# Performance work log

Measured on AMD Instinct MI355X. Metric: run time of the kernel, lower is better.

The kernel has to match this reference:

```python
import jax, jax.numpy as jnp
import numpy as np

K_GRAD = 20        # num_nbrs for gradient operator
K_NORMAL = 10      # knn for normal/basis estimation
GRAD_REG = 1e-3    # grad_reg (lambda)
KERNEL_WIDTH = 1.0 # grad_kernel_width
EPS = 1e-8
N1, N2 = 8192, 8192
CHANNELS = [3, 64, 128, 256]


def knn_idx(pos, k):
    # brute-force kNN incl. self (loop=True, target_to_source)
    sq = jnp.sum(pos * pos, axis=1)
    d2 = sq[:, None] + sq[None, :] - 2.0 * (pos @ pos.T)
    _, idx = jax.lax.top_k(-d2, k)
    return idx  # [N, k]


def estimate_basis(pos, nbr, orientation):
    rel = pos[nbr] - pos[:, None, :]              # [N,k,3]
    cov = jnp.einsum('nki,nkj->nij', rel, rel)    # [N,3,3] local PCA
    _, vecs = jnp.linalg.eigh(cov)                # ascending eigenvalues
    normal, x_basis = vecs[:, :, 0], vecs[:, :, 2]
    sign = jnp.where(jnp.sum(normal * orientation, -1, keepdims=True) < 0.0, -1.0, 1.0)
    normal = normal * sign                        # orient along `orientation`
    y_basis = jnp.cross(normal, x_basis)
    return normal, x_basis, y_basis


def build_grad_div(pos, x_basis, y_basis, nbr):
    # regularized, Gaussian-weighted least-squares fit of a linear function per neighborhood
    rel = pos[nbr] - pos[:, None, :]              # [N,k,3]
    u = jnp.einsum('nkd,nd->nk', rel, x_basis)    # tangent coords
    v = jnp.einsum('nkd,nd->nk', rel, y_basis)
    dist = jnp.sqrt(jnp.sum(rel * rel, -1) + EPS)
    h = jnp.mean(dist, axis=1, keepdims=True)     # per-point bandwidth
    w = jnp.exp(-(dist * dist) / ((KERNEL_WIDTH * h) ** 2 + EPS))
    B = jnp.stack([jnp.ones_like(u), u, v], -1)   # [N,k,3] design matrix
    BtW = jnp.swapaxes(B, 1, 2) * w[:, None, :]   # [N,3,k]
    A = BtW @ B + GRAD_REG * jnp.eye(3, dtype=pos.dtype)
    C = jnp.linalg.solve(A, BtW)                  # [N,3,k] LS coefficients
    Gx, Gy = C[:, 1, :], C[:, 2, :]               # gradient stencils
    basis = jnp.stack([x_basis, y_basis], -1)     # [N,3,2]
    R = jnp.einsum('nda,nkdb->nkab', basis, basis[nbr])  # transport j->i, [N,k,2,2]
    return Gx, Gy, R


def grad_apply(Gx, Gy, nbr, f):
    fn = f[nbr]                                   # [N,k,C]
    return jnp.stack([jnp.einsum('nk,nkc->nc', Gx, fn),
                      jnp.einsum('nk,nkc->nc', Gy, fn)], 1)  # [N,2,C]


def div_apply(Gx, Gy, R, nbr, v):
    vt = jnp.einsum('nkab,nkbc->nkac', R, v[nbr])  # transported neighbor vectors
    return (jnp.einsum('nk,nkc->nc', Gx, vt[:, :, 0]) +
            jnp.einsum('nk,nkc->nc', Gy, vt[:, :, 1]))


def delta_conv(x, v, nbr, Gx, Gy, R, Ws, bs, Wv, bv, centralized):
    xn = x[nbr]
    if centralized:
        xn = xn - x[:, None, :]
    xmax = jnp.max(xn, axis=1)                    # max aggregation
    dv = div_apply(Gx, Gy, R, nbr, v)             # divergence
    Jv = jnp.stack([-v[:, 1], v[:, 0]], 1)        # 90-degree rotation
    cv = div_apply(Gx, Gy, R, nbr, Jv)            # curl = div(J v)
    x_out = jax.nn.relu(jnp.concatenate([xmax, dv, cv], -1) @ Ws + bs)
    if Wv is None:
        return x_out, v                            # last layer: scalar only
    gv = grad_apply(Gx, Gy, nbr, x_out)           # [N,2,Cout]
    vo = jnp.concatenate([v, gv], -1) @ Wv        # channel mix, no bias (equivariant)
    n = jnp.sqrt(jnp.sum(vo * vo, axis=1, keepdims=True) + EPS)
    vo = vo * (jax.nn.relu(n + bv) / (n + EPS))   # norm-gated vector nonlinearity
    return x_out, vo


def _forward(points, als_ppoints, params):
    pos = jnp.concatenate([points, als_ppoints], axis=0)  # [N,3]
    nbr = knn_idx(pos, K_GRAD)
    nbr_n = knn_idx(pos, K_NORMAL)
    _, xb, yb = estimate_basis(pos, nbr_n, orientation=pos)
    Gx, Gy, R = build_grad_div(pos, xb, yb, nbr)
    x = pos
    v = grad_apply(Gx, Gy, nbr, x)                # v = grad @ x
    out = []
    for i, (Ws, bs, Wv, bv) in enumerate(params):
        x, v = delta_conv(x, v, nbr, Gx, Gy, R, Ws, bs, Wv, bv, centralized=(i == 0))
        out.append(x)
    return tuple(out)


def setup_inputs():
    key = jax.random.key(0)
    ks = jax.random.split(key, 8)
    inp = {
        'points': jax.random.normal(ks[0], (N1, 3), jnp.float32),
        'als_ppoints': jax.random.normal(ks[1], (N2, 3), jnp.float32),
    }
    ki = 2
    for i in range(3):
        cin, cout = CHANNELS[i], CHANNELS[i + 1]
        inp[f'Ws{i}'] = jax.random.normal(ks[ki], (3 * cin, cout), jnp.float32) / np.sqrt(3.0 * cin)
        inp[f'bs{i}'] = jnp.zeros((cout,), jnp.float32)
        ki += 1
        if i < 2:
            inp[f'Wv{i}'] = jax.random.normal(ks[ki], (cin + cout, cout), jnp.float32) / np.sqrt(float(cin + cout))
            inp[f'bv{i}'] = jnp.zeros((cout,), jnp.float32)
            ki += 1
    return inp


def reference(points, als_ppoints, Ws0, bs0, Wv0, bv0, Ws1, bs1, Wv1, bv1, Ws2, bs2):
    params = [(Ws0, bs0, Wv0, bv0), (Ws1, bs1, Wv1, bv1), (Ws2, bs2, None, None)]
    return _forward(points, als_ppoints, params)
```

## Files before the change

### kernel.cpp

```cpp
#include <hip/hip_runtime.h>
#include <math.h>

#define NPTS 16384
#define KG 20
#define KN 10
#define KC 6
#define EPSF 1e-8f

#define GDIM 32
#define GL 4.75f
#define CW 0.296875f
#define GINV 3.3684210526f
#define RMAX 6

typedef __attribute__((ext_vector_type(8))) short short8v;
typedef __attribute__((ext_vector_type(4))) float floatx4;

__device__ __forceinline__ unsigned short f2bf(float v) {
  union { float f; unsigned u; } x;
  x.f = v;
  unsigned r = x.u + 0x7FFFu + ((x.u >> 16) & 1u);
  return (unsigned short)(r >> 16);
}

__device__ __forceinline__ float bf2f(unsigned short u) {
  union { unsigned u32; float f; } x;
  x.u32 = (unsigned)u << 16;
  return x.f;
}

#define KNN_INSERT(d2v, iv)                                                 \
  if ((d2v) < dist[KG - 1]) {                                               \
    dist[KG - 1] = (d2v); idx[KG - 1] = (iv);                               \
    _Pragma("unroll")                                                       \
    for (int s_ = KG - 1; s_ > 0; --s_) {                                   \
      if (dist[s_] < dist[s_ - 1]) {                                        \
        float td_ = dist[s_]; dist[s_] = dist[s_ - 1]; dist[s_ - 1] = td_;  \
        int ti_ = idx[s_]; idx[s_] = idx[s_ - 1]; idx[s_ - 1] = ti_;        \
      }                                                                     \
    }                                                                       \
  }

#define KNN_INSERTC(d2v, iv)                                                \
  if ((d2v) < dist[KC - 1]) {                                               \
    dist[KC - 1] = (d2v); idx[KC - 1] = (iv);                               \
    _Pragma("unroll")                                                       \
    for (int s_ = KC - 1; s_ > 0; --s_) {                                   \
      if (dist[s_] < dist[s_ - 1]) {                                        \
        float td_ = dist[s_]; dist[s_] = dist[s_ - 1]; dist[s_ - 1] = td_;  \
        int ti_ = idx[s_]; idx[s_] = idx[s_ - 1]; idx[s_ - 1] = ti_;        \
      }                                                                     \
    }                                                                       \
  }

__device__ __forceinline__ int cell_of(float x) {
  int c = (int)floorf((x + GL) * GINV);
  return min(max(c, 0), GDIM - 1);
}

__global__ __launch_bounds__(256) void posbin_kernel(const float* __restrict__ pts,
                                                     const float* __restrict__ als,
                                                     float4* __restrict__ pos4,
                                                     int* __restrict__ cell_count,
                                                     int* __restrict__ pt_cell) {
  int n = blockIdx.x * 256 + threadIdx.x;
  if (n >= NPTS) return;
  const float* src = (n < 8192) ? (pts + (size_t)n * 3) : (als + (size_t)(n - 8192) * 3);
  float x = src[0], y = src[1], z = src[2];
  pos4[n] = make_float4(x, y, z, 0.f);
  int c = (cell_of(z) * GDIM + cell_of(y)) * GDIM + cell_of(x);
  pt_cell[n] = c;
  atomicAdd(&cell_count[c], 1);
}

__global__ __launch_bounds__(1024) void scan_kernel(const int* __restrict__ cell_count,
                                                    int* __restrict__ cell_start,
                                                    int* __restrict__ cell_cursor) {
  __shared__ int s[1024];
  int tid = threadIdx.x;
  int base = tid * 32;
  int local[32];
  int sum = 0;
#pragma unroll
  for (int i = 0; i < 32; ++i) { local[i] = cell_count[base + i]; sum += local[i]; }
  s[tid] = sum;
  __syncthreads();
  for (int off = 1; off < 1024; off <<= 1) {
    int v = (tid >= off) ? s[tid - off] : 0;
    __syncthreads();
    s[tid] += v;
    __syncthreads();
  }
  int run = s[tid] - sum;
#pragma unroll
  for (int i = 0; i < 32; ++i) {
    cell_start[base + i] = run;
    cell_cursor[base + i] = run;
    run += local[i];
  }
}

__global__ __launch_bounds__(256) void scatter_kernel(const float4* __restrict__ pos4,
                                                      const int* __restrict__ pt_cell,
                                                      int* __restrict__ cell_cursor,
                                                      float4* __restrict__ sorted4,
                                                      int* __restrict__ sortmap) {
  int i = blockIdx.x * 256 + threadIdx.x;
  if (i >= NPTS) return;
  int c = pt_cell[i];
  int dst = atomicAdd(&cell_cursor[c], 1);
  float4 p = pos4[i];
  p.w = __int_as_float(i);
  sorted4[dst] = p;
  sortmap[dst] = i;
}

__global__ __launch_bounds__(256) void knn_grid_kernel(const float4* __restrict__ sorted4,
                                                       const int* __restrict__ cell_start,
                                                       const int* __restrict__ cell_count,
                                                       int* __restrict__ nbr,
                                                       int* __restrict__ fb_list,
                                                       int* __restrict__ fb_count) {
  int lane = threadIdx.x & 63;
  int sub = lane >> 5;
  int sl = lane & 31;
  int qs = blockIdx.x * 8 + (threadIdx.x >> 6) * 2 + sub;
  if (qs >= NPTS) return;
  float4 p = sorted4[qs];
  int cx = cell_of(p.x), cy = cell_of(p.y), cz = cell_of(p.z);
  float dist[KC];
  int idx[KC];
#pragma unroll
  for (int i = 0; i < KC; ++i) { dist[i] = 3.4e38f; idx[i] = 0; }

  {
    int tot = 0;
    int x0 = max(cx - 1, 0), x1 = min(cx + 1, GDIM - 1);
    int zlo = max(cz - 1, 0), zhi = min(cz + 1, GDIM - 1);
    int ylo = max(cy - 1, 0), yhi = min(cy + 1, GDIM - 1);
    for (int z = zlo; z <= zhi; ++z) {
      for (int y = ylo; y <= yhi; ++y) {
        int c0 = (z * GDIM + y) * GDIM + x0;
        int c1 = (z * GDIM + y) * GDIM + x1;
        int beg = cell_start[c0];
        int end = cell_start[c1] + cell_count[c1];
        int off = (sl - tot) & 31;
        for (int j = beg + off; j < end; j += 32) {
          float4 sp = sorted4[j];
          float dx = sp.x - p.x, dy = sp.y - p.y, dz = sp.z - p.z;
          float d2 = dx * dx + dy * dy + dz * dz;
          KNN_INSERTC(d2, j);
        }
        tot += end - beg;
      }
    }
  }
  int done;
  {
    float b2 = CW * CW;
    int cnt = 0;
#pragma unroll
    for (int i = 0; i < KC; ++i) cnt += (dist[i] <= b2) ? 1 : 0;
#pragma unroll
    for (int s = 1; s < 32; s <<= 1) cnt += __shfl_xor(cnt, s, 64);
    done = (cnt >= KG) ? 1 : 0;
  }

  for (int r = 2; r <= RMAX && !done; ++r) {
    int side = 2 * r + 1;
    int nt = side * side;
    float rcp = 1.0f / (float)side;
    for (int t = sl; t < nt; t += 32) {
      int qz = (int)(((float)t + 0.5f) * rcp);
      int dz = qz - r;
      int dy = t - qz * side - r;
      int z = cz + dz, y = cy + dy;
      if (z < 0 || z >= GDIM || y < 0 || y >= GDIM) continue;
      int rowbase = (z * GDIM + y) * GDIM;
      if (dz == -r || dz == r || dy == -r || dy == r) {
        int xa = max(cx - r, 0), xb = min(cx + r, GDIM - 1);
        int beg = cell_start[rowbase + xa];
        int end = cell_start[rowbase + xb] + cell_count[rowbase + xb];
        for (int j = beg; j < end; ++j) {
          float4 sp = sorted4[j];
          float ddx = sp.x - p.x, ddy = sp.y - p.y, ddz = sp.z - p.z;
          float d2 = ddx * ddx + ddy * ddy + ddz * ddz;
          KNN_INSERTC(d2, j);
        }
      } else {
        int x = cx - r;
        if (x >= 0) {
          int c = rowbase + x;
          int beg = cell_start[c], end = beg + cell_count[c];
          for (int j = beg; j < end; ++j) {
            float4 sp = sorted4[j];
            float ddx = sp.x - p.x, ddy = sp.y - p.y, ddz = sp.z - p.z;
            float d2 = ddx * ddx + ddy * ddy + ddz * ddz;
            KNN_INSERTC(d2, j);
          }
        }
        x = cx + r;
        if (x < GDIM) {
          int c = rowbase + x;
          int beg = cell_start[c], end = beg + cell_count[c];
          for (int j = beg; j < end; ++j) {
            float4 sp = sorted4[j];
            float ddx = sp.x - p.x, ddy = sp.y - p.y, ddz = sp.z - p.z;
            float d2 = ddx * ddx + ddy * ddy + ddz * ddz;
            KNN_INSERTC(d2, j);
          }
        }
      }
    }
    float b = CW * (float)r;
    float b2 = b * b;
    int cnt = 0;
#pragma unroll
    for (int i = 0; i < KC; ++i) cnt += (dist[i] <= b2) ? 1 : 0;
#pragma unroll
    for (int s = 1; s < 32; s <<= 1) cnt += __shfl_xor(cnt, s, 64);
    if (cnt >= KG) done = 1;
  }

  int popc = 0, ovf = 0;
  for (int round = 0; round < KG; ++round) {
    unsigned long long key = ((unsigned long long)__float_as_uint(dist[0]) << 14) |
                             (unsigned long long)(unsigned)idx[0];
    unsigned long long m = key;
#pragma unroll
    for (int s = 1; s < 32; s <<= 1) {
      unsigned long long o = __shfl_xor(m, s, 64);
      if (o < m) m = o;
    }
    if (key == m) {
      nbr[(size_t)qs * KG + round] = (int)(m & 0x3FFF);
#pragma unroll
      for (int s = 0; s < KC - 1; ++s) { dist[s] = dist[s + 1]; idx[s] = idx[s + 1]; }
      dist[KC - 1] = 3.4e38f;
      idx[KC - 1] = 0;
      if (++popc == KC) ovf = 1;
    }
  }
#pragma unroll
  for (int s = 1; s < 32; s <<= 1) ovf |= __shfl_xor(ovf, s, 64);
  if ((ovf || !done) && sl == 0) {
    int s = atomicAdd(fb_count, 1);
    fb_list[s] = qs;
  }
}

__global__ __launch_bounds__(256) void knn_fb_kernel(const float4* __restrict__ sorted4,
                                                     const int* __restrict__ fb_list,
                                                     const int* __restrict__ fb_count,
                                                     int* __restrict__ nbr) {
  __shared__ unsigned long long lists[256 * KG];
  __shared__ unsigned long long heads[256];
  __shared__ unsigned long long winner;
  int tid = threadIdx.x;
  int cnt = *fb_count;
  for (int qi = blockIdx.x; qi < cnt; qi += gridDim.x) {
    int t = fb_list[qi];
    float4 p = sorted4[t];
    float dist[KG];
    int idx[KG];
#pragma unroll
    for (int i = 0; i < KG; ++i) { dist[i] = 3.4e38f; idx[i] = 0; }
    int j0 = tid * 64;
    for (int j = j0; j < j0 + 64; ++j) {
      float4 c = sorted4[j];
      float dx = c.x - p.x, dy = c.y - p.y, dz = c.z - p.z;
      float d2 = dx * dx + dy * dy + dz * dz;
      KNN_INSERT(d2, j);
    }
#pragma unroll
    for (int i = 0; i < KG; ++i)
      lists[tid * KG + i] = ((unsigned long long)__float_as_uint(dist[i]) << 22) |
                            ((unsigned long long)(unsigned)idx[i] << 8) |
                            (unsigned long long)tid;
    int hp = 0;
    __syncthreads();
    for (int round = 0; round < KG; ++round) {
      heads[tid] = (hp < KG) ? lists[tid * KG + hp] : ~0ull;
      __syncthreads();
      if (tid < 64) {
        unsigned long long m = heads[tid];
        unsigned long long o = heads[tid + 64];  if (o < m) m = o;
        o = heads[tid + 128]; if (o < m) m = o;
        o = heads[tid + 192]; if (o < m) m = o;
#pragma unroll
        for (int s = 32; s > 0; s >>= 1) {
          unsigned long long x = __shfl_xor(m, s, 64);
          if (x < m) m = x;
        }
        if (tid == 0) winner = m;
      }
      __syncthreads();
      unsigned long long w = winner;
      if (tid == (int)(w & 0xFF)) hp++;
      if (tid == 0) nbr[(size_t)t * KG + round] = (int)((w >> 8) & 0x3FFF);
      __syncthreads();
    }
  }
}

__global__ __launch_bounds__(256) void basis_kernel(const float4* __restrict__ sorted4,
                                                    const int* __restrict__ nbr,
                                                    float4* __restrict__ xb4,
                                                    float4* __restrict__ yb4) {
  int n = blockIdx.x * 256 + threadIdx.x;
  if (n >= NPTS) return;
  float4 p = sorted4[n];
  float c00 = 0, c01 = 0, c02 = 0, c11 = 0, c12 = 0, c22 = 0;
  for (int k = 0; k < KN; ++k) {
    int m = nbr[(size_t)n * KG + k];
    float4 pm = sorted4[m];
    float dx = pm.x - p.x, dy = pm.y - p.y, dz = pm.z - p.z;
    c00 += dx * dx; c01 += dx * dy; c02 += dx * dz;
    c11 += dy * dy; c12 += dy * dz; c22 += dz * dz;
  }
  float nx = 0.f, ny = 0.f, nz = 1.f;
  float p1 = c01 * c01 + c02 * c02 + c12 * c12;
  float qm = (c00 + c11 + c22) * (1.f / 3.f);
  float g0 = c00 - qm, g1 = c11 - qm, g2 = c22 - qm;
  float p2 = g0 * g0 + g1 * g1 + g2 * g2 + 2.f * p1;
  if (p2 > 1e-16f) {
    float pp = sqrtf(p2 * (1.f / 6.f));
    float inv = 1.f / pp;
    float b00 = g0 * inv, b11 = g1 * inv, b22 = g2 * inv;
    float b01 = c01 * inv, b02 = c02 * inv, b12 = c12 * inv;
    float detB = b00 * (b11 * b22 - b12 * b12) - b01 * (b01 * b22 - b12 * b02) +
                 b02 * (b01 * b12 - b11 * b02);
    float r = 0.5f * detB;
    r = fminf(1.f, fmaxf(-1.f, r));
    float phi = acosf(r) * (1.f / 3.f);
    float e1 = qm + 2.f * pp * __cosf(phi);
    float e3 = qm + 2.f * pp * __cosf(phi + 2.0943951023931953f);
    float e2 = 3.f * qm - e1 - e3;
    float a00 = c00 - e1, a11 = c11 - e1, a22 = c22 - e1;
    float f00 = c00 - e2, f11 = c11 - e2, f22 = c22 - e2;
    float u0 = a00 * f00 + c01 * c01 + c02 * c02;
    float u1 = c01 * f00 + a11 * c01 + c12 * c02;
    float u2 = c02 * f00 + c12 * c01 + a22 * c02;
    float v0 = a00 * c01 + c01 * f11 + c02 * c12;
    float v1 = c01 * c01 + a11 * f11 + c12 * c12;
    float v2 = c02 * c01 + c12 * f11 + a22 * c12;
    float w0 = a00 * c02 + c01 * c12 + c02 * f22;
    float w1 = c01 * c02 + a11 * c12 + c12 * f22;
    float w2 = c02 * c02 + c12 * c12 + a22 * f22;
    float nu = u0 * u0 + u1 * u1 + u2 * u2;
    float nv = v0 * v0 + v1 * v1 + v2 * v2;
    float nw = w0 * w0 + w1 * w1 + w2 * w2;
    float bx = u0, by = u1, bz = u2, bn = nu;
    if (nv > bn) { bx = v0; by = v1; bz = v2; bn = nv; }
    if (nw > bn) { bx = w0; by = w1; bz = w2; bn = nw; }
    if (bn > 1e-30f) {
      float s = 1.f / sqrtf(bn);
      nx = bx * s; ny = by * s; nz = bz * s;
    }
  }
  float dotp = nx * p.x + ny * p.y + nz * p.z;
  if (dotp < 0.f) { nx = -nx; ny = -ny; nz = -nz; }
  float ax = fabsf(nx), ay = fabsf(ny), az = fabsf(nz);
  float ex = 0.f, ey = 0.f, ez = 0.f;
  if (ax <= ay && ax <= az) ex = 1.f;
  else if (ay <= az) ey = 1.f;
  else ez = 1.f;
  float tx = ny * ez - nz * ey, ty = nz * ex - nx * ez, tz = nx * ey - ny * ex;
  float tn = 1.f / sqrtf(tx * tx + ty * ty + tz * tz);
  tx *= tn; ty *= tn; tz *= tn;
  float ux = ny * tz - nz * ty, uy = nz * tx - nx * tz, uz = nx * ty - ny * tx;
  xb4[n] = make_float4(tx, ty, tz, 0.f);
  yb4[n] = make_float4(ux, uy, uz, 0.f);
}

__global__ __launch_bounds__(256) void graddiv_kernel(const float4* __restrict__ sorted4,
                                                      const int* __restrict__ nbr,
                                                      const float4* __restrict__ xb4,
                                                      const float4* __restrict__ yb4,
                                                      float* __restrict__ Gx,
                                                      float* __restrict__ Gy,
                                                      float2* __restrict__ C2,
                                                      float* __restrict__ v0) {
  int n = blockIdx.x * 256 + threadIdx.x;
  if (n >= NPTS) return;
  float4 p = sorted4[n], xb = xb4[n], yb = yb4[n];
  float u[KG], vv[KG], w[KG];
  int mm[KG];
  float hsum = 0.f;
#pragma unroll
  for (int k = 0; k < KG; ++k) {
    int m = nbr[(size_t)n * KG + k];
    mm[k] = m;
    float4 pm = sorted4[m];
    float rx = pm.x - p.x, ry = pm.y - p.y, rz = pm.z - p.z;
    u[k] = rx * xb.x + ry * xb.y + rz * xb.z;
    vv[k] = rx * yb.x + ry * yb.y + rz * yb.z;
    float dd = sqrtf(rx * rx + ry * ry + rz * rz + EPSF);
    w[k] = dd; hsum += dd;
  }
  float h = hsum * (1.f / KG);
  float invden = 1.f / (h * h + EPSF);
  float A00 = 0, A01 = 0, A02 = 0, A11 = 0, A12 = 0, A22 = 0;
#pragma unroll
  for (int k = 0; k < KG; ++k) {
    float wk = __expf(-(w[k] * w[k]) * invden);
    w[k] = wk;
    A00 += wk; A01 += wk * u[k]; A02 += wk * vv[k];
    A11 += wk * u[k] * u[k]; A12 += wk * u[k] * vv[k];
    A22 += wk * vv[k] * vv[k];
  }
  A00 += 0.001f; A11 += 0.001f; A22 += 0.001f;
  float det = A00 * (A11 * A22 - A12 * A12) - A01 * (A01 * A22 - A12 * A02) +
              A02 * (A01 * A12 - A11 * A02);
  float idet = 1.f / det;
  float i10 = (A02 * A12 - A01 * A22) * idet;
  float i11 = (A00 * A22 - A02 * A02) * idet;
  float i12 = (A01 * A02 - A00 * A12) * idet;
  float i20 = (A01 * A12 - A02 * A11) * idet;
  float i21 = i12;
  float i22 = (A00 * A11 - A01 * A01) * idet;
  float a0x = 0, a0y = 0, a0z = 0, a1x = 0, a1y = 0, a1z = 0;
#pragma unroll
  for (int k = 0; k < KG; ++k) {
    float gx = w[k] * (i10 + i11 * u[k] + i12 * vv[k]);
    float gy = w[k] * (i20 + i21 * u[k] + i22 * vv[k]);
    Gx[(size_t)n * KG + k] = gx;
    Gy[(size_t)n * KG + k] = gy;
    int m = mm[k];
    float4 pm = sorted4[m];
    a0x += gx * pm.x; a0y += gx * pm.y; a0z += gx * pm.z;
    a1x += gy * pm.x; a1y += gy * pm.y; a1z += gy * pm.z;
    float4 xm = xb4[m], ym = yb4[m];
    float g3x = gx * xb.x + gy * yb.x;
    float g3y = gx * xb.y + gy * yb.y;
    float g3z = gx * xb.z + gy * yb.z;
    float ca = g3x * xm.x + g3y * xm.y + g3z * xm.z;
    float cb = g3x * ym.x + g3y * ym.y + g3z * ym.z;
    C2[(size_t)n * KG + k] = make_float2(ca, cb);
  }
  v0[((size_t)n * 2 + 0) * 3 + 0] = a0x;
  v0[((size_t)n * 2 + 0) * 3 + 1] = a0y;
  v0[((size_t)n * 2 + 0) * 3 + 2] = a0z;
  v0[((size_t)n * 2 + 1) * 3 + 0] = a1x;
  v0[((size_t)n * 2 + 1) * 3 + 1] = a1y;
  v0[((size_t)n * 2 + 1) * 3 + 2] = a1z;
}

template <int CENTRAL>
__global__ __launch_bounds__(256) void feat16_kernel(const float* __restrict__ x, int ldx,
                                                     int cin,
                                                     const float* __restrict__ v,
                                                     const int* __restrict__ nbr,
                                                     const float2* __restrict__ C2,
                                                     unsigned short* __restrict__ feat, int Kp) {
  int per = Kp - 2 * cin;
  int gid = blockIdx.x * 256 + threadIdx.x;
  if (gid >= NPTS * per) return;
  int n = gid / per;
  int c = gid - n * per;
  size_t fb = (size_t)n * Kp;
  if (c >= cin) {
    feat[fb + 3 * cin + (c - cin)] = 0;
    return;
  }
  float xc = x[(size_t)n * ldx + c];
  float xmax = -3.4e38f, dv = 0.f, cv = 0.f;
  for (int k = 0; k < KG; ++k) {
    int m = nbr[(size_t)n * KG + k];
    float2 cc = C2[(size_t)n * KG + k];
    float xm = x[(size_t)m * ldx + c];
    xmax = fmaxf(xmax, CENTRAL ? (xm - xc) : xm);
    float va = v[((size_t)m * 2 + 0) * cin + c];
    float vb = v[((size_t)m * 2 + 1) * cin + c];
    dv += cc.x * va + cc.y * vb;
    cv += cc.y * va - cc.x * vb;
  }
  feat[fb + c] = f2bf(xmax);
  feat[fb + cin + c] = f2bf(dv);
  feat[fb + 2 * cin + c] = f2bf(cv);
}

__global__ __launch_bounds__(256) void feat16v8_kernel(const unsigned short* __restrict__ x,
                                                       int cin,
                                                       const unsigned short* __restrict__ v,
                                                       const int* __restrict__ nbr,
                                                       const float2* __restrict__ C2,
                                                       unsigned short* __restrict__ feat) {
  int per = cin >> 3;
  int gid = blockIdx.x * 256 + threadIdx.x;
  if (gid >= NPTS * per) return;
  int n = gid / per;
  int c8 = (gid - n * per) << 3;
  float xmax[8], dv[8], cv[8];
#pragma unroll
  for (int i = 0; i < 8; ++i) { xmax[i] = -3.4e38f; dv[i] = 0.f; cv[i] = 0.f; }
  const int* nrow = nbr + (size_t)n * KG;
  const float2* crow = C2 + (size_t)n * KG;
#pragma unroll 4
  for (int k = 0; k < KG; ++k) {
    int m = nrow[k];
    float2 cc = crow[k];
    short8v xm = *reinterpret_cast<const short8v*>(x + (size_t)m * cin + c8);
    short8v va = *reinterpret_cast<const short8v*>(v + ((size_t)m * 2 + 0) * cin + c8);
    short8v vb = *reinterpret_cast<const short8v*>(v + ((size_t)m * 2 + 1) * cin + c8);
#pragma unroll
    for (int i = 0; i < 8; ++i) {
      float xf = bf2f((unsigned short)xm[i]);
      float af = bf2f((unsigned short)va[i]);
      float bf = bf2f((unsigned short)vb[i]);
      xmax[i] = fmaxf(xmax[i], xf);
      dv[i] += cc.x * af + cc.y * bf;
      cv[i] += cc.y * af - cc.x * bf;
    }
  }
  size_t fb = (size_t)n * (3 * cin);
  short8v o0, o1, o2;
#pragma unroll
  for (int i = 0; i < 8; ++i) {
    o0[i] = (short)f2bf(xmax[i]);
    o1[i] = (short)f2bf(dv[i]);
    o2[i] = (short)f2bf(cv[i]);
  }
  *reinterpret_cast<short8v*>(&feat[fb + c8]) = o0;
  *reinterpret_cast<short8v*>(&feat[fb + cin + c8]) = o1;
  *reinterpret_cast<short8v*>(&feat[fb + 2 * cin + c8]) = o2;
}

__global__ __launch_bounds__(256) void vin16_kernel(const float* __restrict__ v, int cin,
                                                    const unsigned short* __restrict__ xout,
                                                    int cout,
                                                    const int* __restrict__ nbr,
                                                    const float* __restrict__ Gx,
                                                    const float* __restrict__ Gy,
                                                    unsigned short* __restrict__ vinb, int Kp,
                                                    int total) {
  int gid = blockIdx.x * 256 + threadIdx.x;
  if (gid >= total) return;
  int n = gid / Kp;
  int c = gid - n * Kp;
  int K = cin + cout;
  unsigned short o0, o1;
  if (c < cin) {
    o0 = f2bf(v[((size_t)n * 2 + 0) * cin + c]);
    o1 = f2bf(v[((size_t)n * 2 + 1) * cin + c]);
  } else if (c < K) {
    int cc = c - cin;
    float a0 = 0.f, a1 = 0.f;
    for (int k = 0; k < KG; ++k) {
      int m = nbr[(size_t)n * KG + k];
      float f = bf2f(xout[(size_t)m * cout + cc]);
      a0 += Gx[(size_t)n * KG + k] * f;
      a1 += Gy[(size_t)n * KG + k] * f;
    }
    o0 = f2bf(a0);
    o1 = f2bf(a1);
  } else {
    o0 = 0; o1 = 0;
  }
  vinb[((size_t)n * 2 + 0) * Kp + c] = o0;
  vinb[((size_t)n * 2 + 1) * Kp + c] = o1;
}

__global__ __launch_bounds__(256) void vin16v8_kernel(const unsigned short* __restrict__ v,
                                                      int cin,
                                                      const unsigned short* __restrict__ xout,
                                                      int cout,
                                                      const int* __restrict__ nbr,
                                                      const float* __restrict__ Gx,
                                                      const float* __restrict__ Gy,
                                                      unsigned short* __restrict__ vinb,
                                                      int Kp) {
  int per = Kp >> 3;
  int gid = blockIdx.x * 256 + threadIdx.x;
  if (gid >= NPTS * per) return;
  int n = gid / per;
  int c8 = (gid - n * per) << 3;
  short8v o0, o1;
  if (c8 < cin) {
    o0 = *reinterpret_cast<const short8v*>(v + ((size_t)n * 2 + 0) * cin + c8);
    o1 = *reinterpret_cast<const short8v*>(v + ((size_t)n * 2 + 1) * cin + c8);
  } else {
    int cc8 = c8 - cin;
    float a0[8], a1[8];
#pragma unroll
    for (int i = 0; i < 8; ++i) { a0[i] = 0.f; a1[i] = 0.f; }
    const int* nrow = nbr + (size_t)n * KG;
    const float* gxr = Gx + (size_t)n * KG;
    const float* gyr = Gy + (size_t)n * KG;
#pragma unroll 4
    for (int k = 0; k < KG; ++k) {
      int m = nrow[k];
      float gx = gxr[k], gy = gyr[k];
      short8v f = *reinterpret_cast<const short8v*>(xout + (size_t)m * cout + cc8);
#pragma unroll
      for (int i = 0; i < 8; ++i) {
        float ff = bf2f((unsigned short)f[i]);
        a0[i] += gx * ff;
        a1[i] += gy * ff;
      }
    }
#pragma unroll
    for (int i = 0; i < 8; ++i) {
      o0[i] = (short)f2bf(a0[i]);
      o1[i] = (short)f2bf(a1[i]);
    }
  }
  *reinterpret_cast<short8v*>(&vinb[((size_t)n * 2 + 0) * Kp + c8]) = o0;
  *reinterpret_cast<short8v*>(&vinb[((size_t)n * 2 + 1) * Kp + c8]) = o1;
}

__device__ __forceinline__ void wprep_one(const float* W, unsigned short* Wt, int K, int Kp,
                                          int N, int i) {
  int n = i / Kp, k = i - n * Kp;
  Wt[i] = (k < K) ? f2bf(W[(size_t)k * N + n]) : (unsigned short)0;
}

__global__ __launch_bounds__(256) void wprep_all_kernel(const float* __restrict__ Ws0,
                                                        const float* __restrict__ Wv0,
                                                        const float* __restrict__ Ws1,
                                                        const float* __restrict__ Wv1,
                                                        const float* __restrict__ Ws2,
                                                        unsigned short* __restrict__ Wt_s0,
                                                        unsigned short* __restrict__ Wt_v0,
                                                        unsigned short* __restrict__ Wt_s1,
                                                        unsigned short* __restrict__ Wt_v1,
                                                        unsigned short* __restrict__ Wt_s2) {
  int gid = blockIdx.x * 256 + threadIdx.x;
  if (gid < 2048) wprep_one(Ws0, Wt_s0, 9, 32, 64, gid);
  else if (gid < 8192) wprep_one(Wv0, Wt_v0, 67, 96, 64, gid - 2048);
  else if (gid < 32768) wprep_one(Ws1, Wt_s1, 192, 192, 128, gid - 8192);
  else if (gid < 57344) wprep_one(Wv1, Wt_v1, 192, 192, 128, gid - 32768);
  else if (gid < 155648) wprep_one(Ws2, Wt_s2, 384, 384, 256, gid - 57344);
}

template <int MODE>
__global__ __launch_bounds__(256) void gemm16_kernel(const unsigned short* __restrict__ A,
                                                     const unsigned short* __restrict__ Bt,
                                                     const float* __restrict__ bias,
                                                     float* __restrict__ Cf,
                                                     unsigned short* __restrict__ Cb,
                                                     const int* __restrict__ rowmap,
                                                     int Kp, int Ncol) {
  int lane = threadIdx.x & 63;
  int wave = threadIdx.x >> 6;
  int rowBase = blockIdx.y * 64 + wave * 16;
  int colBase = blockIdx.x * 64;
  int lr = lane & 15;
  int kg = (lane >> 4) * 8;
  floatx4 acc0 = {0.f, 0.f, 0.f, 0.f};
  floatx4 acc1 = acc0, acc2 = acc0, acc3 = acc0;
  const unsigned short* arow = A + (size_t)(rowBase + lr) * Kp + kg;
  const unsigned short* b0p = Bt + (size_t)(colBase + lr) * Kp + kg;
  for (int k0 = 0; k0 < Kp; k0 += 32) {
    short8v a = *reinterpret_cast<const short8v*>(arow + k0);
    short8v b0 = *reinterpret_cast<const short8v*>(b0p + k0);
    short8v b1 = *reinterpret_cast<const short8v*>(b0p + (size_t)16 * Kp + k0);
    short8v b2 = *reinterpret_cast<const short8v*>(b0p + (size_t)32 * Kp + k0);
    short8v b3 = *reinterpret_cast<const short8v*>(b0p + (size_t)48 * Kp + k0);
    acc0 = __builtin_amdgcn_mfma_f32_16x16x32_bf16(a, b0, acc0, 0, 0, 0);
    acc1 = __builtin_amdgcn_mfma_f32_16x16x32_bf16(a, b1, acc1, 0, 0, 0);
    acc2 = __builtin_amdgcn_mfma_f32_16x16x32_bf16(a, b2, acc2, 0, 0, 0);
    acc3 = __builtin_amdgcn_mfma_f32_16x16x32_bf16(a, b3, acc3, 0, 0, 0);
  }
  int rsub = (lane >> 4) * 4;
  floatx4 accs[4] = {acc0, acc1, acc2, acc3};
  int orow[4];
  if (MODE == 0) {
#pragma unroll
    for (int r = 0; r < 4; ++r) orow[r] = rowmap[rowBase + rsub + r];
  }
#pragma unroll
  for (int nb = 0; nb < 4; ++nb) {
    int col = colBase + nb * 16 + lr;
    float bb = bias[col];
    if (MODE == 0) {
#pragma unroll
      for (int r = 0; r < 4; ++r) {
        int row = rowBase + rsub + r;
        float val = fmaxf(accs[nb][r] + bb, 0.f);
        Cf[(size_t)orow[r] * Ncol + col] = val;
        if (Cb) Cb[(size_t)row * Ncol + col] = f2bf(val);
      }
    } else {
#pragma unroll
      for (int pr = 0; pr < 2; ++pr) {
        float a0 = accs[nb][2 * pr], a1 = accs[nb][2 * pr + 1];
        float nrm = sqrtf(a0 * a0 + a1 * a1 + EPSF);
        float s = fmaxf(nrm + bb, 0.f) / (nrm + EPSF);
        int row = rowBase + rsub + 2 * pr;
        Cb[(size_t)row * Ncol + col] = f2bf(a0 * s);
        Cb[(size_t)(row + 1) * Ncol + col] = f2bf(a1 * s);
      }
    }
  }
}

extern "C" void kernel_launch(void* const* d_in, const int* in_sizes, int n_in,
                              void* d_out, int out_size, void* d_ws, size_t ws_size,
                              hipStream_t stream) {
  const float* pts = (const float*)d_in[0];
  const float* als = (const float*)d_in[1];
  const float* Ws0 = (const float*)d_in[2];
  const float* bs0 = (const float*)d_in[3];
  const float* Wv0 = (const float*)d_in[4];
  const float* bv0 = (const float*)d_in[5];
  const float* Ws1 = (const float*)d_in[6];
  const float* bs1 = (const float*)d_in[7];
  const float* Wv1 = (const float*)d_in[8];
  const float* bv1 = (const float*)d_in[9];
  const float* Ws2 = (const float*)d_in[10];
  const float* bs2 = (const float*)d_in[11];

  char* ws = (char*)d_ws;
  float4* pos4 = (float4*)(ws + 0);
  int* nbr = (int*)(ws + 262144);
  float4* xb4 = (float4*)(ws + 1572864);
  float4* yb4 = (float4*)(ws + 1835008);
  float* Gx = (float*)(ws + 2097152);
  float* Gy = (float*)(ws + 3407872);
  float2* C2 = (float2*)(ws + 4718592);
  float* v0f = (float*)(ws + 7340032);
  unsigned short* vb_a = (unsigned short*)(ws + 8388608);
  unsigned short* vb_b = (unsigned short*)(ws + 17825792);
  unsigned short* xb0m = (unsigned short*)(ws + 23068672);
  unsigned short* xb1m = (unsigned short*)(ws + 26214400);
  unsigned short* stg = (unsigned short*)(ws + 31457280);
  char* wtb = ws + 45088768;
  unsigned short* Wt_s0 = (unsigned short*)(wtb + 0);
  unsigned short* Wt_v0 = (unsigned short*)(wtb + 4096);
  unsigned short* Wt_s1 = (unsigned short*)(wtb + 16384);
  unsigned short* Wt_v1 = (unsigned short*)(wtb + 65536);
  unsigned short* Wt_s2 = (unsigned short*)(wtb + 114688);

  char* gws = ws + 46137344;
  int* cell_count = (int*)(gws + 0);
  int* fb_count = (int*)(gws + 131072);
  int* cell_start = (int*)(gws + 135168);
  int* cell_cursor = (int*)(gws + 266240);
  int* pt_cell = (int*)(gws + 397312);
  int* fb_list = (int*)(gws + 462848);
  float4* sorted4 = (float4*)(gws + 532480);
  int* sortmap = (int*)(gws + 794624);

  float* out0 = (float*)d_out;
  float* out1 = out0 + (size_t)NPTS * 64;
  float* out2 = out1 + (size_t)NPTS * 128;

  hipMemsetAsync(cell_count, 0, 131072 + 4, stream);
  posbin_kernel<<<64, 256, 0, stream>>>(pts, als, pos4, cell_count, pt_cell);
  scan_kernel<<<1, 1024, 0, stream>>>(cell_count, cell_start, cell_cursor);
  scatter_kernel<<<64, 256, 0, stream>>>(pos4, pt_cell, cell_cursor, sorted4, sortmap);
  knn_grid_kernel<<<NPTS / 8, 256, 0, stream>>>(sorted4, cell_start, cell_count, nbr, fb_list,
                                                fb_count);
  knn_fb_kernel<<<128, 256, 0, stream>>>(sorted4, fb_list, fb_count, nbr);

  basis_kernel<<<64, 256, 0, stream>>>(sorted4, nbr, xb4, yb4);
  graddiv_kernel<<<64, 256, 0, stream>>>(sorted4, nbr, xb4, yb4, Gx, Gy, C2, v0f);

  wprep_all_kernel<<<608, 256, 0, stream>>>(Ws0, Wv0, Ws1, Wv1, Ws2, Wt_s0, Wt_v0, Wt_s1,
                                            Wt_v1, Wt_s2);

  feat16_kernel<1><<<(NPTS * 26 + 255) / 256, 256, 0, stream>>>((const float*)sorted4, 4, 3,
                                                                v0f, nbr, C2, stg, 32);
  gemm16_kernel<0><<<dim3(1, 256), 256, 0, stream>>>(stg, Wt_s0, bs0, out0, xb0m, sortmap, 32,
                                                     64);
  vin16_kernel<<<(NPTS * 96 + 255) / 256, 256, 0, stream>>>(v0f, 3, xb0m, 64, nbr, Gx, Gy, stg,
                                                            96, NPTS * 96);
  gemm16_kernel<1><<<dim3(1, 512), 256, 0, stream>>>(stg, Wt_v0, bv0, nullptr, vb_b, nullptr,
                                                     96, 64);

  feat16v8_kernel<<<NPTS * 8 / 256, 256, 0, stream>>>(xb0m, 64, vb_b, nbr, C2, stg);
  gemm16_kernel<0><<<dim3(2, 256), 256, 0, stream>>>(stg, Wt_s1, bs1, out1, xb1m, sortmap, 192,
                                                     128);
  vin16v8_kernel<<<NPTS * 24 / 256, 256, 0, stream>>>(vb_b, 64, xb1m, 128, nbr, Gx, Gy, stg,
                                                      192);
  gemm16_kernel<1><<<dim3(2, 512), 256, 0, stream>>>(stg, Wt_v1, bv1, nullptr, vb_a, nullptr,
                                                     192, 128);

  feat16v8_kernel<<<NPTS * 16 / 256, 256, 0, stream>>>(xb1m, 128, vb_a, nbr, C2, stg);
  gemm16_kernel<0><<<dim3(4, 256), 256, 0, stream>>>(stg, Wt_s2, bs2, out2, nullptr, sortmap,
                                                     384, 256);
}
```

Baseline: 292.0 us.

## Fuse weight prep into posbin, unroll kNN scan by two, stage neighbors in LDS

Merges the weight-transpose/bf16 conversion kernel into the point-binning kernel, which removes one launch. Unrolls the grid kNN candidate loop to process two candidates per iteration so more loads are in flight. In feat16v8, a block's neighbor indices and coefficients are loaded cooperatively into shared memory, so threads sharing a point no longer issue redundant global loads. The changes add a __syncthreads and some per-thread branch divergence in the fused kernel.

```diff
diff --git a/kernel.cpp b/kernel.cpp
--- a/kernel.cpp
+++ b/kernel.cpp
@@ -58,19 +58,37 @@
   return min(max(c, 0), GDIM - 1);
 }
 
-__global__ __launch_bounds__(256) void posbin_kernel(const float* __restrict__ pts,
-                                                     const float* __restrict__ als,
-                                                     float4* __restrict__ pos4,
-                                                     int* __restrict__ cell_count,
-                                                     int* __restrict__ pt_cell) {
-  int n = blockIdx.x * 256 + threadIdx.x;
-  if (n >= NPTS) return;
-  const float* src = (n < 8192) ? (pts + (size_t)n * 3) : (als + (size_t)(n - 8192) * 3);
-  float x = src[0], y = src[1], z = src[2];
-  pos4[n] = make_float4(x, y, z, 0.f);
-  int c = (cell_of(z) * GDIM + cell_of(y)) * GDIM + cell_of(x);
-  pt_cell[n] = c;
-  atomicAdd(&cell_count[c], 1);
+__device__ __forceinline__ void wprep_one(const float* W, unsigned short* Wt, int K, int Kp,
+                                          int N, int i) {
+  int n = i / Kp, k = i - n * Kp;
+  Wt[i] = (k < K) ? f2bf(W[(size_t)k * N + n]) : (unsigned short)0;
+}
+
+__global__ __launch_bounds__(256) void posbin_wprep_kernel(
+    const float* __restrict__ pts, const float* __restrict__ als, float4* __restrict__ pos4,
+    int* __restrict__ cell_count, int* __restrict__ pt_cell,
+    const float* __restrict__ Ws0, const float* __restrict__ Wv0,
+    const float* __restrict__ Ws1, const float* __restrict__ Wv1,
+    const float* __restrict__ Ws2, unsigned short* __restrict__ Wt_s0,
+    unsigned short* __restrict__ Wt_v0, unsigned short* __restrict__ Wt_s1,
+    unsigned short* __restrict__ Wt_v1, unsigned short* __restrict__ Wt_s2) {
+  if (blockIdx.x < 64) {
+    int n = blockIdx.x * 256 + threadIdx.x;
+    if (n >= NPTS) return;
+    const float* src = (n < 8192) ? (pts + (size_t)n * 3) : (als + (size_t)(n - 8192) * 3);
+    float x = src[0], y = src[1], z = src[2];
+    pos4[n] = make_float4(x, y, z, 0.f);
+    int c = (cell_of(z) * GDIM + cell_of(y)) * GDIM + cell_of(x);
+    pt_cell[n] = c;
+    atomicAdd(&cell_count[c], 1);
+  } else {
+    int gid = (blockIdx.x - 64) * 256 + threadIdx.x;
+    if (gid < 2048) wprep_one(Ws0, Wt_s0, 9, 32, 64, gid);
+    else if (gid < 8192) wprep_one(Wv0, Wt_v0, 67, 96, 64, gid - 2048);
+    else if (gid < 32768) wprep_one(Ws1, Wt_s1, 192, 192, 128, gid - 8192);
+    else if (gid < 57344) wprep_one(Wv1, Wt_v1, 192, 192, 128, gid - 32768);
+    else if (gid < 155648) wprep_one(Ws2, Wt_s2, 384, 384, 256, gid - 57344);
+  }
 }
 
 __global__ __launch_bounds__(1024) void scan_kernel(const int* __restrict__ cell_count,
@@ -145,11 +163,16 @@
         int beg = cell_start[c0];
         int end = cell_start[c1] + cell_count[c1];
         int off = (sl - tot) & 31;
-        for (int j = beg + off; j < end; j += 32) {
-          float4 sp = sorted4[j];
-          float dx = sp.x - p.x, dy = sp.y - p.y, dz = sp.z - p.z;
-          float d2 = dx * dx + dy * dy + dz * dz;
-          KNN_INSERTC(d2, j);
+        for (int j = beg + off; j < end; j += 64) {
+          int j1 = j + 32;
+          float4 sp0 = sorted4[j];
+          float4 sp1 = sorted4[(j1 < end) ? j1 : j];
+          float dx0 = sp0.x - p.x, dy0 = sp0.y - p.y, dz0 = sp0.z - p.z;
+          float d20 = dx0 * dx0 + dy0 * dy0 + dz0 * dz0;
+          float dx1 = sp1.x - p.x, dy1 = sp1.y - p.y, dz1 = sp1.z - p.z;
+          float d21 = dx1 * dx1 + dy1 * dy1 + dz1 * dz1;
+          KNN_INSERTC(d20, j);
+          if (j1 < end) { KNN_INSERTC(d21, j1); }
         }
         tot += end - beg;
       }
@@ -486,16 +509,27 @@
                                                        const int* __restrict__ nbr,
                                                        const float2* __restrict__ C2,
                                                        unsigned short* __restrict__ feat) {
+  __shared__ int s_nbr[32 * KG];
+  __shared__ float2 s_c2[32 * KG];
   int per = cin >> 3;
-  int gid = blockIdx.x * 256 + threadIdx.x;
-  if (gid >= NPTS * per) return;
-  int n = gid / per;
-  int c8 = (gid - n * per) << 3;
+  int ppb = 256 / per;
+  int pbase = blockIdx.x * ppb;
+  for (int i = threadIdx.x; i < ppb * KG; i += 256) {
+    int pl = i / KG;
+    int kk = i - pl * KG;
+    size_t src = (size_t)(pbase + pl) * KG + kk;
+    s_nbr[i] = nbr[src];
+    s_c2[i] = C2[src];
+  }
+  __syncthreads();
+  int nl = threadIdx.x / per;
+  int n = pbase + nl;
+  int c8 = (threadIdx.x - nl * per) << 3;
   float xmax[8], dv[8], cv[8];
 #pragma unroll
   for (int i = 0; i < 8; ++i) { xmax[i] = -3.4e38f; dv[i] = 0.f; cv[i] = 0.f; }
-  const int* nrow = nbr + (size_t)n * KG;
-  const float2* crow = C2 + (size_t)n * KG;
+  const int* nrow = s_nbr + nl * KG;
+  const float2* crow = s_c2 + nl * KG;
 #pragma unroll 4
   for (int k = 0; k < KG; ++k) {
     int m = nrow[k];
@@ -607,30 +641,6 @@
   }
   *reinterpret_cast<short8v*>(&vinb[((size_t)n * 2 + 0) * Kp + c8]) = o0;
   *reinterpret_cast<short8v*>(&vinb[((size_t)n * 2 + 1) * Kp + c8]) = o1;
-}
-
-__device__ __forceinline__ void wprep_one(const float* W, unsigned short* Wt, int K, int Kp,
-                                          int N, int i) {
-  int n = i / Kp, k = i - n * Kp;
-  Wt[i] = (k < K) ? f2bf(W[(size_t)k * N + n]) : (unsigned short)0;
-}
-
-__global__ __launch_bounds__(256) void wprep_all_kernel(const float* __restrict__ Ws0,
-                                                        const float* __restrict__ Wv0,
-                                                        const float* __restrict__ Ws1,
-                                                        const float* __restrict__ Wv1,
-                                                        const float* __restrict__ Ws2,
-                                                        unsigned short* __restrict__ Wt_s0,
-                                                        unsigned short* __restrict__ Wt_v0,
-                                                        unsigned short* __restrict__ Wt_s1,
-                                                        unsigned short* __restrict__ Wt_v1,
-                                                        unsigned short* __restrict__ Wt_s2) {
-  int gid = blockIdx.x * 256 + threadIdx.x;
-  if (gid < 2048) wprep_one(Ws0, Wt_s0, 9, 32, 64, gid);
-  else if (gid < 8192) wprep_one(Wv0, Wt_v0, 67, 96, 64, gid - 2048);
-  else if (gid < 32768) wprep_one(Ws1, Wt_s1, 192, 192, 128, gid - 8192);
-  else if (gid < 57344) wprep_one(Wv1, Wt_v1, 192, 192, 128, gid - 32768);
-  else if (gid < 155648) wprep_one(Ws2, Wt_s2, 384, 384, 256, gid - 57344);
 }
 
 template <int MODE>
@@ -747,7 +757,9 @@
   float* out2 = out1 + (size_t)NPTS * 128;
 
   hipMemsetAsync(cell_count, 0, 131072 + 4, stream);
-  posbin_kernel<<<64, 256, 0, stream>>>(pts, als, pos4, cell_count, pt_cell);
+  posbin_wprep_kernel<<<672, 256, 0, stream>>>(pts, als, pos4, cell_count, pt_cell, Ws0, Wv0,
+                                               Ws1, Wv1, Ws2, Wt_s0, Wt_v0, Wt_s1, Wt_v1,
+                                               Wt_s2);
   scan_kernel<<<1, 1024, 0, stream>>>(cell_count, cell_start, cell_cursor);
   scatter_kernel<<<64, 256, 0, stream>>>(pos4, pt_cell, cell_cursor, sorted4, sortmap);
   knn_grid_kernel<<<NPTS / 8, 256, 0, stream>>>(sorted4, cell_start, cell_count, nbr, fb_list,
@@ -756,9 +768,6 @@
 
   basis_kernel<<<64, 256, 0, stream>>>(sorted4, nbr, xb4, yb4);
   graddiv_kernel<<<64, 256, 0, stream>>>(sorted4, nbr, xb4, yb4, Gx, Gy, C2, v0f);
-
-  wprep_all_kernel<<<608, 256, 0, stream>>>(Ws0, Wv0, Ws1, Wv1, Ws2, Wt_s0, Wt_v0, Wt_s1,
-                                            Wt_v1, Wt_s2);
 
   feat16_kernel<1><<<(NPTS * 26 + 255) / 256, 256, 0, stream>>>((const float*)sorted4, 4, 3,
                                                                 v0f, nbr, C2, stg, 32);
```

Measured after the change: 288.2 us. No clear change (-1.3%).
